# Performance work log

Measured on AMD Instinct MI355X. Metric: run time of the kernel, lower is better.

The kernel has to match this reference:

```python
import jax, jax.numpy as jnp
import numpy as np

IN_FEATURES = 512
NUM_KNOTS = 64
XMIN = -3.0
XMAX = 3.0


def setup_inputs() -> dict:
    key = jax.random.key(0)
    kx, kc = jax.random.split(key)
    x = jax.random.normal(kx, (65536, IN_FEATURES), dtype=jnp.float32)
    coeffs = jax.random.normal(kc, (IN_FEATURES, NUM_KNOTS), dtype=jnp.float32) * 0.01
    return {"x": x, "coeffs": coeffs}


def reference(x, coeffs):
    # x: (B, F); coeffs: (F, K). Piecewise-linear spline per feature, summed over features.
    K = coeffs.shape[1]
    t = (x - XMIN) / (XMAX - XMIN) * (K - 1)          # (B, F)
    t0 = jnp.clip(jnp.floor(t).astype(jnp.int32), 0, K - 2)
    w1 = t - t0.astype(t.dtype)
    w0 = 1.0 - w1
    feat_idx = jnp.arange(coeffs.shape[0])[None, :]    # (1, F) broadcast with (B, F) indices
    c0 = coeffs[feat_idx, t0]                          # (B, F) gather
    c1 = coeffs[feat_idx, t0 + 1]
    return jnp.sum(w0 * c0 + w1 * c1, axis=1)          # (B,)
```

## Files before the change

### kernel.cpp

```cpp
#include <hip/hip_runtime.h>


#define TILE_B 64
#define CHUNK_F 128
#define NCHUNK 4
#define LSTRIDE 129
#define FPW 32

__global__ __launch_bounds__(256, 4)
void spline_kernel(const float* __restrict__ x,
                   const float* __restrict__ coeffs,
                   float* __restrict__ out)
{
    __shared__ float ldsX[TILE_B * LSTRIDE];
    __shared__ float ldsR[4 * TILE_B];

    const int t    = threadIdx.x;
    const int lane = t & 63;
    const int w    = t >> 6;
    const long rowBase = (long)blockIdx.x * TILE_B;

    float acc0 = 0.0f, acc1 = 0.0f;

    for (int ch = 0; ch < NCHUNK; ++ch) {
        const int cbase = ch * CHUNK_F;
        __syncthreads();
        #pragma unroll
        for (int s = 0; s < 8; ++s) {
            int i4 = s * 256 + t;
            int r  = i4 >> 5;
            int c4 = i4 & 31;
            const float4 v = *reinterpret_cast<const float4*>(
                x + (rowBase + r) * 512 + cbase + c4 * 4);
            float* dst = &ldsX[r * LSTRIDE + c4 * 4];
            dst[0] = v.x; dst[1] = v.y; dst[2] = v.z; dst[3] = v.w;
        }
        __syncthreads();
        #pragma unroll 8
        for (int j = 0; j < FPW; ++j) {
            const int fc = w * FPW + j;
            const int f  = cbase + fc;
            const float cr = coeffs[f * 64 + lane];
            const float xv = ldsX[lane * LSTRIDE + fc];
            const float tt  = (xv + 3.0f) * 10.5f;
            float t0f = floorf(tt);
            t0f = fminf(fmaxf(t0f, 0.0f), 62.0f);
            const int t0 = (int)t0f;
            const float c0 = __shfl(cr, t0, 64);
            const float c1 = __shfl(cr, t0 + 1, 64);
            const float w1 = tt - t0f;
            if (j & 1) acc1 += c0 + w1 * (c1 - c0);
            else       acc0 += c0 + w1 * (c1 - c0);
        }
    }

    ldsR[w * TILE_B + lane] = acc0 + acc1;
    __syncthreads();
    if (t < TILE_B) {
        float r = ldsR[t] + ldsR[TILE_B + t] + ldsR[2 * TILE_B + t] + ldsR[3 * TILE_B + t];
        out[rowBase + t] = r;
    }
}

extern "C" void kernel_launch(void* const* d_in, const int* in_sizes, int n_in,
                              void* d_out, int out_size, void* d_ws, size_t ws_size,
                              hipStream_t stream) {
    const float* x      = (const float*)d_in[0];
    const float* coeffs = (const float*)d_in[1];
    float* out = (float*)d_out;
    (void)in_sizes; (void)n_in; (void)out_size; (void)d_ws; (void)ws_size;

    dim3 grid(65536 / TILE_B);
    dim3 block(256);
    spline_kernel<<<grid, block, 0, stream>>>(x, coeffs, out);
}
```

Before: 34.82 us.

## Prefetch next x chunk into registers and pack bf16 coefficient pairs for single bpermute

```diff
diff --git a/kernel.cpp b/kernel.cpp
--- a/kernel.cpp
+++ b/kernel.cpp
@@ -1,4 +1,5 @@
 #include <hip/hip_runtime.h>
+#include <stdint.h>
 
 
 #define TILE_B 64
@@ -6,6 +7,11 @@
 #define NCHUNK 4
 #define LSTRIDE 129
 #define FPW 32
+
+__device__ __forceinline__ uint32_t bf16_rne(float v) {
+    uint32_t u = __float_as_uint(v);
+    return (u + 0x7fffu + ((u >> 16) & 1u)) >> 16;
+}
 
 __global__ __launch_bounds__(256, 4)
 void spline_kernel(const float* __restrict__ x,
@@ -19,46 +25,82 @@
     const int lane = t & 63;
     const int w    = t >> 6;
     const long rowBase = (long)blockIdx.x * TILE_B;
+    const float* xb = x + rowBase * 512;
+
+    float4 pf[8];
+
+    #pragma unroll
+    for (int s = 0; s < 8; ++s) {
+        const int i4 = s * 256 + t;
+        const int r = i4 >> 5, c4 = i4 & 31;
+        pf[s] = *reinterpret_cast<const float4*>(xb + r * 512 + c4 * 4);
+    }
+    #pragma unroll
+    for (int s = 0; s < 8; ++s) {
+        const int i4 = s * 256 + t;
+        const int r = i4 >> 5, c4 = i4 & 31;
+        float* dst = &ldsX[r * LSTRIDE + c4 * 4];
+        dst[0] = pf[s].x; dst[1] = pf[s].y; dst[2] = pf[s].z; dst[3] = pf[s].w;
+    }
+    __syncthreads();
 
     float acc0 = 0.0f, acc1 = 0.0f;
 
     for (int ch = 0; ch < NCHUNK; ++ch) {
-        const int cbase = ch * CHUNK_F;
-        __syncthreads();
-        #pragma unroll
-        for (int s = 0; s < 8; ++s) {
-            int i4 = s * 256 + t;
-            int r  = i4 >> 5;
-            int c4 = i4 & 31;
-            const float4 v = *reinterpret_cast<const float4*>(
-                x + (rowBase + r) * 512 + cbase + c4 * 4);
-            float* dst = &ldsX[r * LSTRIDE + c4 * 4];
-            dst[0] = v.x; dst[1] = v.y; dst[2] = v.z; dst[3] = v.w;
+        if (ch < NCHUNK - 1) {
+            const int cb = (ch + 1) * CHUNK_F;
+            #pragma unroll
+            for (int s = 0; s < 8; ++s) {
+                const int i4 = s * 256 + t;
+                const int r = i4 >> 5, c4 = i4 & 31;
+                pf[s] = *reinterpret_cast<const float4*>(xb + r * 512 + cb + c4 * 4);
+            }
+        }
+        const int   cbase = ch * CHUNK_F;
+        const float* ldx  = &ldsX[lane * LSTRIDE + w * FPW];
+        #pragma unroll 4
+        for (int j = 0; j < FPW; j += 2) {
+            const int f = cbase + w * FPW + j;
+            const float c0a = coeffs[f * 64 + lane];
+            const float c1a = coeffs[f * 64 + ((lane + 1) & 63)];
+            const float c0b = coeffs[f * 64 + 64 + lane];
+            const float c1b = coeffs[f * 64 + 64 + ((lane + 1) & 63)];
+            const uint32_t pa = (bf16_rne(c0a) << 16) | bf16_rne(c1a - c0a);
+            const uint32_t pb = (bf16_rne(c0b) << 16) | bf16_rne(c1b - c0b);
+
+            const float xva = ldx[j];
+            const float xvb = ldx[j + 1];
+
+            const float tta  = (xva + 3.0f) * 10.5f;
+            const float t0fa = fminf(fmaxf(floorf(tta), 0.0f), 62.0f);
+            const uint32_t ga = (uint32_t)__builtin_amdgcn_ds_bpermute(((int)t0fa) << 2, (int)pa);
+            const float w1a  = tta - t0fa;
+            acc0 += __uint_as_float(ga & 0xffff0000u) + w1a * __uint_as_float(ga << 16);
+
+            const float ttb  = (xvb + 3.0f) * 10.5f;
+            const float t0fb = fminf(fmaxf(floorf(ttb), 0.0f), 62.0f);
+            const uint32_t gb = (uint32_t)__builtin_amdgcn_ds_bpermute(((int)t0fb) << 2, (int)pb);
+            const float w1b  = ttb - t0fb;
+            acc1 += __uint_as_float(gb & 0xffff0000u) + w1b * __uint_as_float(gb << 16);
         }
         __syncthreads();
-        #pragma unroll 8
-        for (int j = 0; j < FPW; ++j) {
-            const int fc = w * FPW + j;
-            const int f  = cbase + fc;
-            const float cr = coeffs[f * 64 + lane];
-            const float xv = ldsX[lane * LSTRIDE + fc];
-            const float tt  = (xv + 3.0f) * 10.5f;
-            float t0f = floorf(tt);
-            t0f = fminf(fmaxf(t0f, 0.0f), 62.0f);
-            const int t0 = (int)t0f;
-            const float c0 = __shfl(cr, t0, 64);
-            const float c1 = __shfl(cr, t0 + 1, 64);
-            const float w1 = tt - t0f;
-            if (j & 1) acc1 += c0 + w1 * (c1 - c0);
-            else       acc0 += c0 + w1 * (c1 - c0);
+        if (ch < NCHUNK - 1) {
+            #pragma unroll
+            for (int s = 0; s < 8; ++s) {
+                const int i4 = s * 256 + t;
+                const int r = i4 >> 5, c4 = i4 & 31;
+                float* dst = &ldsX[r * LSTRIDE + c4 * 4];
+                dst[0] = pf[s].x; dst[1] = pf[s].y; dst[2] = pf[s].z; dst[3] = pf[s].w;
+            }
         }
+        __syncthreads();
     }
 
     ldsR[w * TILE_B + lane] = acc0 + acc1;
     __syncthreads();
     if (t < TILE_B) {
-        float r = ldsR[t] + ldsR[TILE_B + t] + ldsR[2 * TILE_B + t] + ldsR[3 * TILE_B + t];
-        out[rowBase + t] = r;
+        out[rowBase + t] = ldsR[t] + ldsR[TILE_B + t]
+                         + ldsR[2 * TILE_B + t] + ldsR[3 * TILE_B + t];
     }
 }
 
```

After: 46.30 us. 1.33x slower.
